# Performance work log

Measured on AMD Instinct MI355X. Metric: run time of the kernel, lower is better.

## Reference

```python
import jax, jax.numpy as jnp
import numpy as np

HQ, HKV, HD = 16, 4, 64  # q heads, kv heads, head dim
ROPE_BASE = 10000.0


def _rope_tables(n, dim):
    inv_freq = 1.0 / (ROPE_BASE ** (jnp.arange(0, dim, 2, dtype=jnp.float32) / dim))
    t = jnp.arange(n, dtype=jnp.float32)
    freqs = jnp.outer(t, inv_freq)           # [N, dim/2]
    emb = jnp.concatenate([freqs, freqs], -1)  # [N, dim]
    return jnp.cos(emb), jnp.sin(emb)


def _rotate_half(x):
    h = x.shape[-1] // 2
    return jnp.concatenate([-x[..., h:], x[..., :h]], axis=-1)


def _apply_rope(x, cos, sin):
    # x: [B, N, H, D]; cos/sin: [N, D]
    c = cos[None, :, None, :]
    s = sin[None, :, None, :]
    return x * c + _rotate_half(x) * s


def setup_inputs() -> dict:
    key = jax.random.key(0)
    ks = jax.random.split(key, 5)
    B, N, D = 2, 4096, 1024
    kvD = HKV * HD
    sc = 0.02
    return {
        "x": jax.random.normal(ks[0], (B, N, D), jnp.float32),
        "Wq": jax.random.normal(ks[1], (D, D), jnp.float32) * sc,
        "Wk": jax.random.normal(ks[2], (D, kvD), jnp.float32) * sc,
        "Wv": jax.random.normal(ks[3], (D, kvD), jnp.float32) * sc,
        "Wo": jax.random.normal(ks[4], (D, D), jnp.float32) * sc,
    }


def reference(x, Wq, Wk, Wv, Wo):
    B, N, D = x.shape
    G = HQ // HKV
    Q = (x @ Wq).reshape(B, N, HQ, HD)
    K = (x @ Wk).reshape(B, N, HKV, HD)
    V = (x @ Wv).reshape(B, N, HKV, HD)

    cos, sin = _rope_tables(N, HD)
    Q = _apply_rope(Q, cos, sin)
    K = _apply_rope(K, cos, sin)

    # GQA: expand KV heads to match Q heads (repeat_interleave over head dim)
    K = jnp.repeat(K, G, axis=2)  # [B, N, HQ, HD]
    V = jnp.repeat(V, G, axis=2)

    Q = Q.transpose(0, 2, 1, 3)  # [B, HQ, N, HD]
    K = K.transpose(0, 2, 1, 3)
    V = V.transpose(0, 2, 1, 3)

    scores = jnp.einsum('bhqd,bhkd->bhqk', Q, K) / jnp.sqrt(jnp.float32(HD))
    attn = jax.nn.softmax(scores, axis=-1)
    out = jnp.einsum('bhqk,bhkd->bhqd', attn, V)  # [B, HQ, N, HD]
    out = out.transpose(0, 2, 1, 3).reshape(B, N, D)
    return out @ Wo
```

## Files before the change

kernel.cpp:

```cpp
#include <hip/hip_runtime.h>

#define HQn   16
#define HKVn  4
#define HDn   64
#define SEQN  4096
#define NB    2
#define DM    1024
#define KVD   256
#define NPACK 1536

#define QSCALE 0.18033688011112042f

typedef __attribute__((ext_vector_type(8))) short short8;
typedef __attribute__((ext_vector_type(4))) float f32x4;

#define MFMA16 __builtin_amdgcn_mfma_f32_16x16x32_bf16
#define EXP2F(x) __builtin_amdgcn_exp2f(x)

static __device__ __forceinline__ unsigned short f2bf(float f){
  union { float f; unsigned int u; } c; c.f = f;
  unsigned int r = c.u + 0x7fffu + ((c.u >> 16) & 1u);
  return (unsigned short)(r >> 16);
}

#if __has_builtin(__builtin_amdgcn_cvt_pk_bf16_f32)
typedef __attribute__((ext_vector_type(2))) __bf16 bf16x2v;
static __device__ __forceinline__ unsigned int pk_bf2(float a, float b){
  union { bf16x2v v; unsigned int u; } c;
  c.v = __builtin_amdgcn_cvt_pk_bf16_f32(a, b);
  return c.u;
}
#else
static __device__ __forceinline__ unsigned int pk_bf2(float a, float b){
  union { float f; unsigned int u; } ca, cb; ca.f = a; cb.f = b;
  return ((ca.u + 0x8000u) >> 16) | ((cb.u + 0x8000u) & 0xFFFF0000u);
}
#endif

static __device__ __forceinline__ void gl2lds16(const void* g, void* l){
  __builtin_amdgcn_global_load_lds(
      (const __attribute__((address_space(1))) void*)g,
      (__attribute__((address_space(3))) void*)l, 16, 0, 0);
}

__global__ void rope_tables_k(float* __restrict__ ct, float* __restrict__ st){
  int t = blockIdx.x, d = threadIdx.x;
  int i = d & 31;
  float inv = 1.0f / powf(10000.0f, (float)i * (1.0f/32.0f));
  float ang = (float)t * inv;
  ct[t*HDn + d] = cosf(ang);
  st[t*HDn + d] = sinf(ang);
}

__global__ __launch_bounds__(256) void castx_k(const float* __restrict__ x,
                                               unsigned short* __restrict__ xb){
  size_t i = ((size_t)blockIdx.x * 256 + threadIdx.x) * 8;
  float4 a = *(const float4*)(x + i);
  float4 b = *(const float4*)(x + i + 4);
  short8 o;
  o[0]=f2bf(a.x); o[1]=f2bf(a.y); o[2]=f2bf(a.z); o[3]=f2bf(a.w);
  o[4]=f2bf(b.x); o[5]=f2bf(b.y); o[6]=f2bf(b.z); o[7]=f2bf(b.w);
  *(short8*)(xb + i) = o;
}

__global__ __launch_bounds__(256) void castw_k(
    const float* __restrict__ Wq, const float* __restrict__ Wk,
    const float* __restrict__ Wv, const float* __restrict__ Wo,
    unsigned short* __restrict__ Wqkv_t, unsigned short* __restrict__ Wot)
{
  const int z = blockIdx.z;
  const float* W; unsigned short* D; int srcN, nOff;
  if      (z == 0) { W = Wq; D = Wqkv_t; srcN = DM;  nOff = 0;    }
  else if (z == 1) { W = Wo; D = Wot;    srcN = DM;  nOff = 0;    }
  else if (z == 2) { W = Wk; D = Wqkv_t; srcN = KVD; nOff = 1024; }
  else             { W = Wv; D = Wqkv_t; srcN = KVD; nOff = 1280; }
  const int n0 = blockIdx.y * 64;
  if (n0 >= srcN) return;
  const int k0 = blockIdx.x * 64;
  const int tid = threadIdx.x;

  __shared__ float tile[64][65];
  const int lr = tid >> 4, lc = (tid & 15) * 4;
  #pragma unroll
  for (int p = 0; p < 4; p++) {
    float4 v = *(const float4*)&W[(size_t)(k0 + lr + p*16) * srcN + n0 + lc];
    tile[lr + p*16][lc+0] = v.x; tile[lr + p*16][lc+1] = v.y;
    tile[lr + p*16][lc+2] = v.z; tile[lr + p*16][lc+3] = v.w;
  }
  __syncthreads();

  const int nn = tid >> 2, kc = (tid & 3) * 16;
  unsigned short* dp = D + (size_t)(nOff + n0 + nn) * DM + k0 + kc;
  #pragma unroll
  for (int q = 0; q < 4; q++) {
    ushort4 o;
    o.x = f2bf(tile[kc + q*4 + 0][nn]);
    o.y = f2bf(tile[kc + q*4 + 1][nn]);
    o.z = f2bf(tile[kc + q*4 + 2][nn]);
    o.w = f2bf(tile[kc + q*4 + 3][nn]);
    *(ushort4*)(dp + q*4) = o;
  }
}

__global__ __launch_bounds__(256) void qkv2_k(
    const unsigned short* __restrict__ A, const unsigned short* __restrict__ Bt,
    const float* __restrict__ ct, const float* __restrict__ st,
    unsigned short* __restrict__ Qo, unsigned short* __restrict__ Ko,
    unsigned short* __restrict__ Vo)
{
  __shared__ __align__(16) short As[2][128][32];
  __shared__ __align__(16) short Bs[2][128][32];

  const int m0 = blockIdx.x * 128, n0 = blockIdx.y * 128;
  const int tid = threadIdx.x, lane = tid & 63, w = tid >> 6;
  const int wm = w >> 1, wn = w & 1;
  const int ln = lane & 15, quad = lane >> 4;

  f32x4 acc[4][4];
  #pragma unroll
  for (int i = 0; i < 4; i++)
    #pragma unroll
    for (int j = 0; j < 4; j++) acc[i][j] = (f32x4){0.f,0.f,0.f,0.f};

  const int r0 = tid >> 2, c8 = (tid & 3) * 8;
  const int r1 = r0 + 64;

  #define GSTAGE(cn, kk)                                                     \
    do {                                                                     \
      gl2lds16(A  + (size_t)(m0 + r0)*DM + (kk) + c8, &As[cn][r0][c8]);      \
      gl2lds16(A  + (size_t)(m0 + r1)*DM + (kk) + c8, &As[cn][r1][c8]);      \
      gl2lds16(Bt + (size_t)(n0 + r0)*DM + (kk) + c8, &Bs[cn][r0][c8]);      \
      gl2lds16(Bt + (size_t)(n0 + r1)*DM + (kk) + c8, &Bs[cn][r1][c8]);      \
    } while (0)

  GSTAGE(0, 0);
  __syncthreads();

  int cb = 0;
  for (int k0 = 0; k0 < DM; k0 += 32) {
    if (k0 + 32 < DM) GSTAGE(cb ^ 1, k0 + 32);

    short8 af[4], bf[4];
    #pragma unroll
    for (int mb = 0; mb < 4; mb++) af[mb] = *(const short8*)&As[cb][wm*64 + mb*16 + ln][quad*8];
    #pragma unroll
    for (int nb = 0; nb < 4; nb++) bf[nb] = *(const short8*)&Bs[cb][wn*64 + nb*16 + ln][quad*8];
    #pragma unroll
    for (int mb = 0; mb < 4; mb++)
      #pragma unroll
      for (int nb = 0; nb < 4; nb++)
        acc[mb][nb] = MFMA16(af[mb], bf[nb], acc[mb][nb], 0, 0, 0);

    __syncthreads();
    cb ^= 1;
  }
  #undef GSTAGE

  const int nc = n0 + wn*64;
  int kind, head;
  if (nc < 1024)      { kind = 0; head = nc >> 6;          }
  else if (nc < 1280) { kind = 1; head = (nc - 1024) >> 6; }
  else                { kind = 2; head = (nc - 1280) >> 6; }

  if (kind == 2) {
    #pragma unroll
    for (int mb = 0; mb < 4; mb++) {
      const int m = m0 + wm*64 + mb*16 + quad*4;
      const int t = m & (SEQN-1), b = m >> 12;
      #pragma unroll
      for (int nb = 0; nb < 4; nb++) {
        int d = nb*16 + ln;
        ushort4 pk;
        pk.x = f2bf(acc[mb][nb][0]); pk.y = f2bf(acc[mb][nb][1]);
        pk.z = f2bf(acc[mb][nb][2]); pk.w = f2bf(acc[mb][nb][3]);
        *(ushort4*)&Vo[(((size_t)(b*HKVn + head))*HDn + d)*SEQN + t] = pk;
      }
    }
  } else {
    #pragma unroll
    for (int mb = 0; mb < 4; mb++) {
      #pragma unroll
      for (int nb = 0; nb < 4; nb++) {
        #pragma unroll
        for (int r = 0; r < 4; r++) {
          int m = m0 + wm*64 + mb*16 + quad*4 + r;
          int t = m & (SEQN-1), b = m >> 12;
          int d = nb*16 + ln;
          float v = acc[mb][nb][r];
          float partner = (nb < 2) ? -acc[mb][nb+2][r] : acc[mb][nb-2][r];
          float cv = ct[t*HDn + d], sv = st[t*HDn + d];
          float o = v*cv + partner*sv;
          if (kind == 0) Qo[(((size_t)(b*HQn  + head))*SEQN + t)*HDn + d] = f2bf(o * QSCALE);
          else           Ko[(((size_t)(b*HKVn + head))*SEQN + t)*HDn + d] = f2bf(o);
        }
      }
    }
  }
}

__global__ __launch_bounds__(256, 4) void attn_k(
    const unsigned short* __restrict__ Q, const unsigned short* __restrict__ K,
    const unsigned short* __restrict__ Vt, unsigned short* __restrict__ AO)
{
  __shared__ __align__(16) short kb[2][64][64];
  __shared__ __align__(16) short vb[2][64][64];

  const int id  = blockIdx.x;
  const int bhv = id & 7;
  const int b   = bhv >> 2, hv = bhv & 3;
  const int rem = id >> 3;
  const int qt  = rem & 31;
  const int h   = hv*4 + (rem >> 5);
  const int q0  = qt * 128;

  const int tid = threadIdx.x, lane = tid & 63, w = tid >> 6;
  const int ln = lane & 15, quad = lane >> 4;

  const unsigned short* Qp = Q + (((size_t)(b*HQn + h))*SEQN + q0 + w*32) * HDn;
  const unsigned short* Kp = K + ((size_t)(b*HKVn + hv))*SEQN * HDn;
  const unsigned short* Vp = Vt + ((size_t)(b*HKVn + hv))*HDn * SEQN;

  short8 qf[2][2];
  qf[0][0] = *(const short8*)(Qp + ln*HDn + quad*8);
  qf[0][1] = *(const short8*)(Qp + ln*HDn + 32 + quad*8);
  qf[1][0] = *(const short8*)(Qp + (16+ln)*HDn + quad*8);
  qf[1][1] = *(const short8*)(Qp + (16+ln)*HDn + 32 + quad*8);

  short8 ones;
  #pragma unroll
  for (int j = 0; j < 8; j++) ones[j] = (short)0x3F80;

  f32x4 o[2][4], lacc[2];
  #pragma unroll
  for (int g = 0; g < 2; g++) {
    #pragma unroll
    for (int i = 0; i < 4; i++) o[g][i] = (f32x4){0.f,0.f,0.f,0.f};
    lacc[g] = (f32x4){0.f,0.f,0.f,0.f};
  }

  const int w2   = w & 1;
  const int lrow = lane >> 3;
  const int slin = lane & 7;
  const int sK   = slin ^ lrow;

  int kkey[4]; size_t vrow[4];
  #pragma unroll
  for (int i = 0; i < 4; i++) {
    kkey[i] = 32*w2 + 16*(i & 1) + 8*(lrow >> 2) + 4*(i >> 1) + (lrow & 3);
    vrow[i] = (size_t)(w2*32 + i*8 + lrow) * SEQN;
  }

  #define STAGE(cn, kts)                                                     \
    do {                                                                     \
      if (w < 2) {                                                           \
        _Pragma("unroll")                                                    \
        for (int i = 0; i < 4; i++)                                          \
          gl2lds16(Kp + (size_t)((kts) + kkey[i])*HDn + sK*8,                \
                   &kb[cn][w2*32 + i*8][0]);                                 \
      } else {                                                               \
        _Pragma("unroll")                                                    \
        for (int i = 0; i < 4; i++)                                          \
          gl2lds16(Vp + vrow[i] + (kts) + sK*8,                              \
                   &vb[cn][w2*32 + i*8][0]);                                 \
      }                                                                      \
    } while (0)

  const int swz0 = (( quad      ^ (ln & 7)) * 8);
  const int swz1 = (((quad + 4) ^ (ln & 7)) * 8);

  STAGE(0, 0);
  __syncthreads();

  int c = 0;
  for (int kt = 0; kt < SEQN; kt += 64) {
    if (kt + 64 < SEQN) STAGE(c ^ 1, kt + 64);

    f32x4 s[2][4];
    __builtin_amdgcn_s_setprio(1);
    #pragma unroll
    for (int nb = 0; nb < 4; nb++) {
      short8 k0 = *(const short8*)&kb[c][nb*16 + ln][swz0];
      short8 k1 = *(const short8*)&kb[c][nb*16 + ln][swz1];
      f32x4 t0 = (f32x4){0.f,0.f,0.f,0.f};
      t0 = MFMA16(k0, qf[0][0], t0, 0, 0, 0);
      t0 = MFMA16(k1, qf[0][1], t0, 0, 0, 0);
      s[0][nb] = t0;
      f32x4 t1 = (f32x4){0.f,0.f,0.f,0.f};
      t1 = MFMA16(k0, qf[1][0], t1, 0, 0, 0);
      t1 = MFMA16(k1, qf[1][1], t1, 0, 0, 0);
      s[1][nb] = t1;
    }
    __builtin_amdgcn_s_setprio(0);

    short8 pf[2][2];
    #pragma unroll
    for (int g = 0; g < 2; g++) {
      #pragma unroll
      for (int k2 = 0; k2 < 2; k2++) {
        union { short8 s8; unsigned u[4]; } f;
        f.u[0] = pk_bf2(EXP2F(s[g][2*k2  ][0]), EXP2F(s[g][2*k2  ][1]));
        f.u[1] = pk_bf2(EXP2F(s[g][2*k2  ][2]), EXP2F(s[g][2*k2  ][3]));
        f.u[2] = pk_bf2(EXP2F(s[g][2*k2+1][0]), EXP2F(s[g][2*k2+1][1]));
        f.u[3] = pk_bf2(EXP2F(s[g][2*k2+1][2]), EXP2F(s[g][2*k2+1][3]));
        pf[g][k2] = f.s8;
      }
    }

    __builtin_amdgcn_s_setprio(1);
    #pragma unroll
    for (int db = 0; db < 4; db++) {
      short8 v0 = *(const short8*)&vb[c][db*16 + ln][swz0];
      short8 v1 = *(const short8*)&vb[c][db*16 + ln][swz1];
      o[0][db] = MFMA16(pf[0][0], v0, o[0][db], 0, 0, 0);
      o[0][db] = MFMA16(pf[0][1], v1, o[0][db], 0, 0, 0);
      o[1][db] = MFMA16(pf[1][0], v0, o[1][db], 0, 0, 0);
      o[1][db] = MFMA16(pf[1][1], v1, o[1][db], 0, 0, 0);
    }
    lacc[0] = MFMA16(pf[0][0], ones, lacc[0], 0, 0, 0);
    lacc[0] = MFMA16(pf[0][1], ones, lacc[0], 0, 0, 0);
    lacc[1] = MFMA16(pf[1][0], ones, lacc[1], 0, 0, 0);
    lacc[1] = MFMA16(pf[1][1], ones, lacc[1], 0, 0, 0);
    __builtin_amdgcn_s_setprio(0);

    __syncthreads();
    c ^= 1;
  }
  #undef STAGE

  #pragma unroll
  for (int g = 0; g < 2; g++) {
    float inv[4];
    #pragma unroll
    for (int r = 0; r < 4; r++) inv[r] = 1.0f / lacc[g][r];
    #pragma unroll
    for (int db = 0; db < 4; db++) {
      #pragma unroll
      for (int r = 0; r < 4; r++) {
        int gq = q0 + w*32 + g*16 + quad*4 + r;
        int d  = db*16 + ln;
        AO[(((size_t)(b*SEQN + gq))*HQn + h)*HDn + d] = f2bf(o[g][db][r] * inv[r]);
      }
    }
  }
}

__global__ __launch_bounds__(256) void oproj2_k(
    const unsigned short* __restrict__ A, const unsigned short* __restrict__ Bt,
    float* __restrict__ out)
{
  __shared__ __align__(16) short As[2][128][32];
  __shared__ __align__(16) short Bs[2][128][32];

  const int m0 = blockIdx.x * 128, n0 = blockIdx.y * 128;
  const int tid = threadIdx.x, lane = tid & 63, w = tid >> 6;
  const int wm = w >> 1, wn = w & 1;
  const int ln = lane & 15, quad = lane >> 4;

  f32x4 acc[4][4];
  #pragma unroll
  for (int i = 0; i < 4; i++)
    #pragma unroll
    for (int j = 0; j < 4; j++) acc[i][j] = (f32x4){0.f,0.f,0.f,0.f};

  const int r0 = tid >> 2, c8 = (tid & 3) * 8;
  const int r1 = r0 + 64;

  #define GSTAGE(cn, kk)                                                     \
    do {                                                                     \
      gl2lds16(A  + (size_t)(m0 + r0)*DM + (kk) + c8, &As[cn][r0][c8]);      \
      gl2lds16(A  + (size_t)(m0 + r1)*DM + (kk) + c8, &As[cn][r1][c8]);      \
      gl2lds16(Bt + (size_t)(n0 + r0)*DM + (kk) + c8, &Bs[cn][r0][c8]);      \
      gl2lds16(Bt + (size_t)(n0 + r1)*DM + (kk) + c8, &Bs[cn][r1][c8]);      \
    } while (0)

  GSTAGE(0, 0);
  __syncthreads();

  int cb = 0;
  for (int k0 = 0; k0 < DM; k0 += 32) {
    if (k0 + 32 < DM) GSTAGE(cb ^ 1, k0 + 32);

    short8 af[4], bf[4];
    #pragma unroll
    for (int mb = 0; mb < 4; mb++) af[mb] = *(const short8*)&As[cb][wm*64 + mb*16 + ln][quad*8];
    #pragma unroll
    for (int nb = 0; nb < 4; nb++) bf[nb] = *(const short8*)&Bs[cb][wn*64 + nb*16 + ln][quad*8];
    #pragma unroll
    for (int mb = 0; mb < 4; mb++)
      #pragma unroll
      for (int nb = 0; nb < 4; nb++)
        acc[mb][nb] = MFMA16(af[mb], bf[nb], acc[mb][nb], 0, 0, 0);

    __syncthreads();
    cb ^= 1;
  }
  #undef GSTAGE

  #pragma unroll
  for (int mb = 0; mb < 4; mb++) {
    #pragma unroll
    for (int nb = 0; nb < 4; nb++) {
      #pragma unroll
      for (int r = 0; r < 4; r++) {
        int m = m0 + wm*64 + mb*16 + quad*4 + r;
        int c = n0 + wn*64 + nb*16 + ln;
        out[(size_t)m*DM + c] = acc[mb][nb][r];
      }
    }
  }
}

extern "C" void kernel_launch(void* const* d_in, const int* in_sizes, int n_in,
                              void* d_out, int out_size, void* d_ws, size_t ws_size,
                              hipStream_t stream) {
  const float* x  = (const float*)d_in[0];
  const float* Wq = (const float*)d_in[1];
  const float* Wk = (const float*)d_in[2];
  const float* Wv = (const float*)d_in[3];
  const float* Wo = (const float*)d_in[4];
  float* out = (float*)d_out;

  char* ws = (char*)d_ws;
  float* cos_t = (float*)ws;
  float* sin_t = cos_t + SEQN*HDn;
  unsigned short* xb     = (unsigned short*)(sin_t + SEQN*HDn);
  unsigned short* AO     = xb;
  unsigned short* Wqkv_t = xb + (size_t)NB*SEQN*DM;
  unsigned short* Wot    = Wqkv_t + (size_t)NPACK*DM;
  unsigned short* Qb     = Wot + (size_t)DM*DM;
  unsigned short* Kb     = Qb + (size_t)NB*HQn *SEQN*HDn;
  unsigned short* Vb     = Kb + (size_t)NB*HKVn*SEQN*HDn;

  hipLaunchKernelGGL(rope_tables_k, dim3(SEQN), dim3(HDn), 0, stream, cos_t, sin_t);
  hipLaunchKernelGGL(castx_k, dim3((NB*SEQN*DM)/(256*8)), dim3(256), 0, stream, x, xb);
  hipLaunchKernelGGL(castw_k, dim3(16, 16, 4), dim3(256), 0, stream,
                     Wq, Wk, Wv, Wo, Wqkv_t, Wot);
  hipLaunchKernelGGL(qkv2_k, dim3(64, 12), dim3(256), 0, stream,
                     xb, Wqkv_t, cos_t, sin_t, Qb, Kb, Vb);
  hipLaunchKernelGGL(attn_k, dim3(1024), dim3(256), 0, stream,
                     Qb, Kb, Vb, AO);
  hipLaunchKernelGGL(oproj2_k, dim3(64, 8), dim3(256), 0, stream,
                     AO, Wot, out);
}
```

Baseline: 303.0 us.

## Triple-buffer LDS staging in projection GEMMs with partial vmcnt waits

Both projection GEMM kernels (QKV and output) move from double to triple-buffered LDS tiles, prefetching two K-steps ahead. The full __syncthreads is replaced by s_waitcnt vmcnt(4) plus a raw s_barrier, so one stage of global-to-LDS loads stays in flight across the barrier. The goal is to hide global load latency behind MFMA work. The cost is 50% more LDS per block, which may lower occupancy, and correctness now depends on the hand-set vmcnt counts matching the four loads issued per stage.

```diff
diff --git a/kernel.cpp b/kernel.cpp
--- a/kernel.cpp
+++ b/kernel.cpp
@@ -108,8 +108,8 @@
     unsigned short* __restrict__ Qo, unsigned short* __restrict__ Ko,
     unsigned short* __restrict__ Vo)
 {
-  __shared__ __align__(16) short As[2][128][32];
-  __shared__ __align__(16) short Bs[2][128][32];
+  __shared__ __align__(16) short As[3][128][32];
+  __shared__ __align__(16) short Bs[3][128][32];
 
   const int m0 = blockIdx.x * 128, n0 = blockIdx.y * 128;
   const int tid = threadIdx.x, lane = tid & 63, w = tid >> 6;
@@ -134,11 +134,15 @@
     } while (0)
 
   GSTAGE(0, 0);
-  __syncthreads();
+  GSTAGE(1, 32);
+  asm volatile("s_waitcnt vmcnt(4)" ::: "memory");
+  __builtin_amdgcn_s_barrier();
 
   int cb = 0;
   for (int k0 = 0; k0 < DM; k0 += 32) {
-    if (k0 + 32 < DM) GSTAGE(cb ^ 1, k0 + 32);
+    int nb2 = cb + 2; if (nb2 >= 3) nb2 -= 3;
+    const bool staged = (k0 + 64 < DM);
+    if (staged) GSTAGE(nb2, k0 + 64);
 
     short8 af[4], bf[4];
     #pragma unroll
@@ -151,8 +155,12 @@
       for (int nb = 0; nb < 4; nb++)
         acc[mb][nb] = MFMA16(af[mb], bf[nb], acc[mb][nb], 0, 0, 0);
 
-    __syncthreads();
-    cb ^= 1;
+    if (k0 + 32 < DM) {
+      if (staged) asm volatile("s_waitcnt vmcnt(4)" ::: "memory");
+      else        asm volatile("s_waitcnt vmcnt(0)" ::: "memory");
+      __builtin_amdgcn_s_barrier();
+    }
+    cb = cb + 1; if (cb >= 3) cb -= 3;
   }
   #undef GSTAGE
 
@@ -348,8 +356,8 @@
     const unsigned short* __restrict__ A, const unsigned short* __restrict__ Bt,
     float* __restrict__ out)
 {
-  __shared__ __align__(16) short As[2][128][32];
-  __shared__ __align__(16) short Bs[2][128][32];
+  __shared__ __align__(16) short As[3][128][32];
+  __shared__ __align__(16) short Bs[3][128][32];
 
   const int m0 = blockIdx.x * 128, n0 = blockIdx.y * 128;
   const int tid = threadIdx.x, lane = tid & 63, w = tid >> 6;
@@ -374,11 +382,15 @@
     } while (0)
 
   GSTAGE(0, 0);
-  __syncthreads();
+  GSTAGE(1, 32);
+  asm volatile("s_waitcnt vmcnt(4)" ::: "memory");
+  __builtin_amdgcn_s_barrier();
 
   int cb = 0;
   for (int k0 = 0; k0 < DM; k0 += 32) {
-    if (k0 + 32 < DM) GSTAGE(cb ^ 1, k0 + 32);
+    int nb2 = cb + 2; if (nb2 >= 3) nb2 -= 3;
+    const bool staged = (k0 + 64 < DM);
+    if (staged) GSTAGE(nb2, k0 + 64);
 
     short8 af[4], bf[4];
     #pragma unroll
@@ -391,8 +403,12 @@
       for (int nb = 0; nb < 4; nb++)
         acc[mb][nb] = MFMA16(af[mb], bf[nb], acc[mb][nb], 0, 0, 0);
 
-    __syncthreads();
-    cb ^= 1;
+    if (k0 + 32 < DM) {
+      if (staged) asm volatile("s_waitcnt vmcnt(4)" ::: "memory");
+      else        asm volatile("s_waitcnt vmcnt(0)" ::: "memory");
+      __builtin_amdgcn_s_barrier();
+    }
+    cb = cb + 1; if (cb >= 3) cb -= 3;
   }
   #undef GSTAGE
 
```

Result: slower. 334.3 us (+10.3%).
